# Kernel tuning notes

Measured on AMD Instinct MI355X. Metric: run time of the kernel, lower is better.

## Reference

```python
import jax, jax.numpy as jnp
import numpy as np

N_NODES = 50000
N_EDGES = 1600000
IN_DIM = 512
OUT_DIM = 256


def setup_inputs() -> dict:
    key = jax.random.key(0)
    k1, k2, k3, k4, k5, k6 = jax.random.split(key, 6)
    inputs = jax.random.normal(k1, (N_NODES, IN_DIM), dtype=jnp.float32)
    edge_row = jax.random.randint(k2, (N_EDGES,), 0, N_NODES, dtype=jnp.int32)
    edge_col = jax.random.randint(k3, (N_EDGES,), 0, N_NODES, dtype=jnp.int32)
    edge_val = jax.random.uniform(k4, (N_EDGES,), dtype=jnp.float32)
    stdv = 1.0 / np.sqrt(OUT_DIM)
    weight = jax.random.uniform(k5, (IN_DIM, OUT_DIM), dtype=jnp.float32, minval=-stdv, maxval=stdv)
    bias = jax.random.uniform(k6, (OUT_DIM,), dtype=jnp.float32, minval=-stdv, maxval=stdv)
    return {"inputs": inputs, "edge_row": edge_row, "edge_col": edge_col,
            "edge_val": edge_val, "weight": weight, "bias": bias}


def reference(inputs, edge_row, edge_col, edge_val, weight, bias):
    # dense GEMM: [N, in] @ [in, out] -> [N, out]
    support = inputs @ weight
    # SpMM: out[r] += val * support[c] for each edge (r, c, val)
    gathered = edge_val[:, None] * support[edge_col]  # [E, out]
    output = jax.ops.segment_sum(gathered, edge_row, num_segments=N_NODES)
    return output + bias
```

## Files before the change

kernel.cpp:

```cpp
#include <hip/hip_runtime.h>

#define N_NODES 50000
#define N_EDGES 1600000
#define IN_DIM 512
#define OUT_DIM 256

#define BM 64
#define BN 256
#define BK 32
#define APAD 8
#define LDA (BK + APAD)

#define RPB   128
#define NBKT  391
#define CHUNK 4096
#define CAP   5120

typedef unsigned int u32;
typedef unsigned short u16;
typedef short bf16x8 __attribute__((ext_vector_type(8)));
typedef float f32x4 __attribute__((ext_vector_type(4)));

__device__ __forceinline__ float bf_to_f(u16 u) { return __uint_as_float(((u32)u) << 16); }
__device__ __forceinline__ u16 f_to_bf(float f) {
    u32 u = __float_as_uint(f);
    u32 r = (u + 0x7fffu + ((u >> 16) & 1u)) >> 16;
    return (u16)r;
}

__global__ __launch_bounds__(256) void scatter1(const int* __restrict__ er,
                                                const int* __restrict__ ec,
                                                const float* __restrict__ ev,
                                                int* __restrict__ cursor,
                                                int2* __restrict__ tmp) {
    __shared__ int  hcnt[NBKT];
    __shared__ int  loff[NBKT];
    __shared__ int  gbase[NBKT];
    __shared__ int  sc[512];
    __shared__ int2 estage[CHUNK];
    __shared__ u16  bslot[CHUNK];

    const int t = threadIdx.x;
    const int base = blockIdx.x * CHUNK;
    const int nedge = min(CHUNK, N_EDGES - base);

    for (int k = t; k < NBKT; k += 256) hcnt[k] = 0;
    __syncthreads();

    int w0[16], w1[16], rk[16];
    #pragma unroll
    for (int j = 0; j < 16; ++j) {
        const int i = j * 256 + t;
        rk[j] = -1;
        if (i < nedge) {
            const int e = base + i;
            const int r = er[e];
            const int bk = r >> 7;
            w0[j] = ec[e] | ((r & 127) << 16) | (bk << 23);
            w1[j] = __float_as_int(ev[e]);
            rk[j] = atomicAdd(&hcnt[bk], 1);
        }
    }
    __syncthreads();

    sc[t]       = (t < NBKT) ? hcnt[t] : 0;
    sc[t + 256] = (t + 256 < NBKT) ? hcnt[t + 256] : 0;
    __syncthreads();
    #pragma unroll
    for (int off = 1; off < 512; off <<= 1) {
        const int a0 = (t >= off) ? sc[t - off] : 0;
        const int a1 = sc[t + 256 - off];
        __syncthreads();
        sc[t] += a0;
        sc[t + 256] += a1;
        __syncthreads();
    }
    if (t < NBKT)       loff[t]       = sc[t] - hcnt[t];
    if (t + 256 < NBKT) loff[t + 256] = sc[t + 256] - hcnt[t + 256];

    if (t < NBKT && hcnt[t] > 0)
        gbase[t] = t * CAP + atomicAdd(&cursor[t], hcnt[t]);
    if (t + 256 < NBKT && hcnt[t + 256] > 0)
        gbase[t + 256] = (t + 256) * CAP + atomicAdd(&cursor[t + 256], hcnt[t + 256]);
    __syncthreads();

    #pragma unroll
    for (int j = 0; j < 16; ++j) {
        if (rk[j] >= 0) {
            const int bk = ((u32)w0[j]) >> 23;
            const int s = loff[bk] + rk[j];
            estage[s] = make_int2(w0[j], w1[j]);
            bslot[s]  = (u16)bk;
        }
    }
    __syncthreads();

    for (int s = t; s < nedge; s += 256) {
        const int bk = bslot[s];
        const int2 e2 = estage[s];
        const int gpos = gbase[bk] + (s - loff[bk]);
        if (gpos < (bk + 1) * CAP)
            tmp[gpos] = e2;
    }
}

__global__ __launch_bounds__(256) void scatter2(const int* __restrict__ cursor,
                                                const int2* __restrict__ tmp,
                                                int* __restrict__ row_ptr,
                                                int2* __restrict__ sedge) {
    __shared__ int sc[512];
    __shared__ int orig[512];
    __shared__ int rcnt[RPB];
    __shared__ int rsc[RPB];
    __shared__ int rcur[RPB];
    const int t = threadIdx.x;
    const int b = blockIdx.x;

    const int c0 = (t < NBKT) ? min(cursor[t], CAP) : 0;
    const int c1 = (t + 256 < NBKT) ? min(cursor[t + 256], CAP) : 0;
    sc[t] = c0;       orig[t] = c0;
    sc[t + 256] = c1; orig[t + 256] = c1;
    __syncthreads();
    #pragma unroll
    for (int off = 1; off < 512; off <<= 1) {
        const int a0 = (t >= off) ? sc[t - off] : 0;
        const int a1 = sc[t + 256 - off];
        __syncthreads();
        sc[t] += a0;
        sc[t + 256] += a1;
        __syncthreads();
    }
    const int gb = sc[b] - orig[b];
    const int n  = orig[b];
    const int2* src = tmp + (size_t)b * CAP;

    if (b == 0 && t == 0) row_ptr[N_NODES] = N_EDGES;

    if (t < RPB) rcnt[t] = 0;
    __syncthreads();
    for (int i = t; i < n; i += 256)
        atomicAdd(&rcnt[(((u32)src[i].x) >> 16) & 127], 1);
    __syncthreads();

    if (t < RPB) rsc[t] = rcnt[t];
    __syncthreads();
    #pragma unroll
    for (int off = 1; off < RPB; off <<= 1) {
        int a = 0;
        if (t < RPB && t >= off) a = rsc[t - off];
        __syncthreads();
        if (t < RPB) rsc[t] += a;
        __syncthreads();
    }
    if (t < RPB) {
        const int excl = rsc[t] - rcnt[t];
        rcur[t] = gb + excl;
        const int row = b * RPB + t;
        if (row < N_NODES) row_ptr[row] = gb + excl;
    }
    __syncthreads();

    for (int i = t; i < n; i += 256) {
        const int2 e2 = src[i];
        const int rloc = (((u32)e2.x) >> 16) & 127;
        const int pos = atomicAdd(&rcur[rloc], 1);
        sedge[pos] = make_int2(e2.x & 0xFFFF, e2.y);
    }
}

__global__ __launch_bounds__(256) void wcvt_zero(const float* __restrict__ W,
                                                 u16* __restrict__ WT,
                                                 int* __restrict__ cursor) {
    if (blockIdx.x < 2) {
        const int i = blockIdx.x * 256 + threadIdx.x;
        if (i < NBKT) cursor[i] = 0;
    }
    const int n  = threadIdx.x;
    const int k0 = blockIdx.x * 4;
    ushort4 o;
    o.x = f_to_bf(W[(size_t)(k0 + 0) * OUT_DIM + n]);
    o.y = f_to_bf(W[(size_t)(k0 + 1) * OUT_DIM + n]);
    o.z = f_to_bf(W[(size_t)(k0 + 2) * OUT_DIM + n]);
    o.w = f_to_bf(W[(size_t)(k0 + 3) * OUT_DIM + n]);
    *(ushort4*)(WT + (size_t)n * IN_DIM + k0) = o;
}

__global__ __launch_bounds__(256) void gemm_mfma(const float* __restrict__ X,
                                                 const u16* __restrict__ WT,
                                                 u16* __restrict__ Sb) {
    __shared__ u16 As[BM * LDA];
    __shared__ u16 Bs[BN * LDA];

    const int tid  = threadIdx.x;
    const int wave = tid >> 6;
    const int lane = tid & 63;
    const int r0   = blockIdx.x * BM;
    const int wn   = wave * 64;
    const int l15  = lane & 15;
    const int quad = lane >> 4;

    f32x4 acc[4][4];
    #pragma unroll
    for (int i = 0; i < 4; ++i)
        #pragma unroll
        for (int j = 0; j < 4; ++j) acc[i][j] = (f32x4)0.f;

    const int arow = tid >> 2;
    const int akp  = (tid & 3) * 8;
    const int xrow = min(r0 + arow, N_NODES - 1);
    const float* xsrc = X + (size_t)xrow * IN_DIM + akp;
    const int brow = tid >> 1;
    const int bkp  = (tid & 1) * 16;
    const u16* bsrc  = WT + (size_t)brow * IN_DIM + bkp;
    const u16* bsrc2 = bsrc + (size_t)128 * IN_DIM;

    float4 fA0 = *(const float4*)(xsrc + 0);
    float4 fA1 = *(const float4*)(xsrc + 4);
    uint4  rB0 = *(const uint4*)(bsrc + 0);
    uint4  rB1 = *(const uint4*)(bsrc + 8);
    uint4  rB2 = *(const uint4*)(bsrc2 + 0);
    uint4  rB3 = *(const uint4*)(bsrc2 + 8);

    for (int kc = 0; kc < IN_DIM; kc += BK) {
        {
            ushort4 p0, p1;
            p0.x = f_to_bf(fA0.x); p0.y = f_to_bf(fA0.y); p0.z = f_to_bf(fA0.z); p0.w = f_to_bf(fA0.w);
            p1.x = f_to_bf(fA1.x); p1.y = f_to_bf(fA1.y); p1.z = f_to_bf(fA1.z); p1.w = f_to_bf(fA1.w);
            *(ushort4*)&As[arow * LDA + akp + 0] = p0;
            *(ushort4*)&As[arow * LDA + akp + 4] = p1;
            *(uint4*)&Bs[brow * LDA + bkp + 0] = rB0;
            *(uint4*)&Bs[brow * LDA + bkp + 8] = rB1;
            *(uint4*)&Bs[(brow + 128) * LDA + bkp + 0] = rB2;
            *(uint4*)&Bs[(brow + 128) * LDA + bkp + 8] = rB3;
        }
        __syncthreads();

        if (kc + BK < IN_DIM) {
            fA0 = *(const float4*)(xsrc + kc + BK + 0);
            fA1 = *(const float4*)(xsrc + kc + BK + 4);
            rB0 = *(const uint4*)(bsrc + kc + BK + 0);
            rB1 = *(const uint4*)(bsrc + kc + BK + 8);
            rB2 = *(const uint4*)(bsrc2 + kc + BK + 0);
            rB3 = *(const uint4*)(bsrc2 + kc + BK + 8);
        }

        bf16x8 af[4], bfr[4];
        #pragma unroll
        for (int mt = 0; mt < 4; ++mt)
            af[mt] = *(const bf16x8*)&As[(mt * 16 + l15) * LDA + quad * 8];
        #pragma unroll
        for (int nt = 0; nt < 4; ++nt)
            bfr[nt] = *(const bf16x8*)&Bs[(wn + nt * 16 + l15) * LDA + quad * 8];
        #pragma unroll
        for (int mt = 0; mt < 4; ++mt)
            #pragma unroll
            for (int nt = 0; nt < 4; ++nt)
                acc[mt][nt] = __builtin_amdgcn_mfma_f32_16x16x32_bf16(
                    af[mt], bfr[nt], acc[mt][nt], 0, 0, 0);
        __syncthreads();
    }

    #pragma unroll
    for (int mt = 0; mt < 4; ++mt) {
        #pragma unroll
        for (int r = 0; r < 4; ++r) {
            const int grow = r0 + mt * 16 + quad * 4 + r;
            if (grow < N_NODES) {
                u16* dst = Sb + (size_t)grow * OUT_DIM + wn + l15;
                #pragma unroll
                for (int nt = 0; nt < 4; ++nt)
                    dst[nt * 16] = f_to_bf(acc[mt][nt][r]);
            }
        }
    }
}

__global__ __launch_bounds__(256) void csr_spmm(const int* __restrict__ row_ptr,
                                                const int2* __restrict__ sedge,
                                                const u16* __restrict__ Sb,
                                                const float* __restrict__ bias,
                                                float* __restrict__ out,
                                                int rbase) {
    const int wave = threadIdx.x >> 6;
    const int lane = threadIdx.x & 63;
    const int r = rbase + blockIdx.x * 4 + wave;
    if (r >= N_NODES) return;

    const int start = row_ptr[r];
    const int end   = row_ptr[r + 1];

    float4 acc = *(const float4*)(bias + lane * 4);
    const u16* sbase = Sb + lane * 4;

    int e = start;
    for (; e + 16 <= end; e += 16) {
        int2 ed[16];
        #pragma unroll
        for (int j = 0; j < 16; ++j) ed[j] = sedge[e + j];

        ushort4 sv[16];
        #pragma unroll
        for (int j = 0; j < 16; ++j)
            sv[j] = *(const ushort4*)(sbase + (size_t)ed[j].x * OUT_DIM);

        #pragma unroll
        for (int j = 0; j < 16; ++j) {
            const float vj = __int_as_float(ed[j].y);
            acc.x += vj * bf_to_f(sv[j].x);
            acc.y += vj * bf_to_f(sv[j].y);
            acc.z += vj * bf_to_f(sv[j].z);
            acc.w += vj * bf_to_f(sv[j].w);
        }
    }
    if (e < end) {
        int2 ed[16];
        #pragma unroll
        for (int j = 0; j < 16; ++j)
            ed[j] = sedge[min(e + j, end - 1)];
        #pragma unroll
        for (int j = 0; j < 16; ++j)
            if (e + j >= end) ed[j].y = 0;

        ushort4 sv[16];
        #pragma unroll
        for (int j = 0; j < 16; ++j)
            sv[j] = *(const ushort4*)(sbase + (size_t)ed[j].x * OUT_DIM);

        #pragma unroll
        for (int j = 0; j < 16; ++j) {
            const float vj = __int_as_float(ed[j].y);
            acc.x += vj * bf_to_f(sv[j].x);
            acc.y += vj * bf_to_f(sv[j].y);
            acc.z += vj * bf_to_f(sv[j].z);
            acc.w += vj * bf_to_f(sv[j].w);
        }
    }

    *(float4*)(out + (size_t)r * OUT_DIM + lane * 4) = acc;
}

extern "C" void kernel_launch(void* const* d_in, const int* in_sizes, int n_in,
                              void* d_out, int out_size, void* d_ws, size_t ws_size,
                              hipStream_t stream) {
    const float* X    = (const float*)d_in[0];
    const int*   er   = (const int*)d_in[1];
    const int*   ec   = (const int*)d_in[2];
    const float* ev   = (const float*)d_in[3];
    const float* W    = (const float*)d_in[4];
    const float* bias = (const float*)d_in[5];
    float* out        = (float*)d_out;

    char* ws = (char*)d_ws;
    u16*  Sb      = (u16*) (ws);
    int2* tmp     = (int2*)(ws);
    int*  cursor  = (int*) (ws + 16100000);
    int2* sedge   = (int2*)(ws + 25600000);
    u16*  WT      = (u16*) (ws + 38400000);
    int*  row_ptr = (int*) (ws + 38662144);

    hipLaunchKernelGGL(wcvt_zero, dim3(IN_DIM / 4), dim3(256), 0, stream,
                       W, WT, cursor);
    hipLaunchKernelGGL(scatter1, dim3((N_EDGES + CHUNK - 1) / CHUNK), dim3(256), 0,
                       stream, er, ec, ev, cursor, tmp);
    hipLaunchKernelGGL(scatter2, dim3(NBKT), dim3(256), 0, stream,
                       cursor, tmp, row_ptr, sedge);
    hipLaunchKernelGGL(gemm_mfma, dim3((N_NODES + BM - 1) / BM), dim3(256), 0,
                       stream, X, WT, Sb);
    hipLaunchKernelGGL(csr_spmm, dim3(25000 / 4), dim3(256), 0, stream,
                       row_ptr, sedge, Sb, bias, out, 0);
    hipLaunchKernelGGL(csr_spmm, dim3(25000 / 4), dim3(256), 0, stream,
                       row_ptr, sedge, Sb, bias, out, 25000);
}
```

Baseline: 357.0 us.

## Fuse CSR bucket sort pass with GEMM in one heterogeneous launch

Merges the second scatter kernel (per-bucket row sort and row_ptr build) and the bf16 MFMA GEMM into one grid. The first NBKT blocks do the sort and the rest do GEMM tiles, so the two independent stages can overlap and one launch boundary disappears. Because tmp previously aliased the Sb buffer, the workspace is relaid out so tmp, WT, row_ptr and cursor no longer overlap Sb. The cost is a larger workspace footprint and shared memory sized for the GEMM in every block.

```diff
diff --git a/kernel.cpp b/kernel.cpp
--- a/kernel.cpp
+++ b/kernel.cpp
@@ -14,6 +14,7 @@
 #define RPB   128
 #define NBKT  391
 #define CHUNK 4096
+#define EPT   16
 #define CAP   5120
 
 typedef unsigned int u32;
@@ -47,9 +48,9 @@
     for (int k = t; k < NBKT; k += 256) hcnt[k] = 0;
     __syncthreads();
 
-    int w0[16], w1[16], rk[16];
+    int w0[EPT], w1[EPT], rk[EPT];
     #pragma unroll
-    for (int j = 0; j < 16; ++j) {
+    for (int j = 0; j < EPT; ++j) {
         const int i = j * 256 + t;
         rk[j] = -1;
         if (i < nedge) {
@@ -85,7 +86,7 @@
     __syncthreads();
 
     #pragma unroll
-    for (int j = 0; j < 16; ++j) {
+    for (int j = 0; j < EPT; ++j) {
         if (rk[j] >= 0) {
             const int bk = ((u32)w0[j]) >> 23;
             const int s = loff[bk] + rk[j];
@@ -101,70 +102,6 @@
         const int gpos = gbase[bk] + (s - loff[bk]);
         if (gpos < (bk + 1) * CAP)
             tmp[gpos] = e2;
-    }
-}
-
-__global__ __launch_bounds__(256) void scatter2(const int* __restrict__ cursor,
-                                                const int2* __restrict__ tmp,
-                                                int* __restrict__ row_ptr,
-                                                int2* __restrict__ sedge) {
-    __shared__ int sc[512];
-    __shared__ int orig[512];
-    __shared__ int rcnt[RPB];
-    __shared__ int rsc[RPB];
-    __shared__ int rcur[RPB];
-    const int t = threadIdx.x;
-    const int b = blockIdx.x;
-
-    const int c0 = (t < NBKT) ? min(cursor[t], CAP) : 0;
-    const int c1 = (t + 256 < NBKT) ? min(cursor[t + 256], CAP) : 0;
-    sc[t] = c0;       orig[t] = c0;
-    sc[t + 256] = c1; orig[t + 256] = c1;
-    __syncthreads();
-    #pragma unroll
-    for (int off = 1; off < 512; off <<= 1) {
-        const int a0 = (t >= off) ? sc[t - off] : 0;
-        const int a1 = sc[t + 256 - off];
-        __syncthreads();
-        sc[t] += a0;
-        sc[t + 256] += a1;
-        __syncthreads();
-    }
-    const int gb = sc[b] - orig[b];
-    const int n  = orig[b];
-    const int2* src = tmp + (size_t)b * CAP;
-
-    if (b == 0 && t == 0) row_ptr[N_NODES] = N_EDGES;
-
-    if (t < RPB) rcnt[t] = 0;
-    __syncthreads();
-    for (int i = t; i < n; i += 256)
-        atomicAdd(&rcnt[(((u32)src[i].x) >> 16) & 127], 1);
-    __syncthreads();
-
-    if (t < RPB) rsc[t] = rcnt[t];
-    __syncthreads();
-    #pragma unroll
-    for (int off = 1; off < RPB; off <<= 1) {
-        int a = 0;
-        if (t < RPB && t >= off) a = rsc[t - off];
-        __syncthreads();
-        if (t < RPB) rsc[t] += a;
-        __syncthreads();
-    }
-    if (t < RPB) {
-        const int excl = rsc[t] - rcnt[t];
-        rcur[t] = gb + excl;
-        const int row = b * RPB + t;
-        if (row < N_NODES) row_ptr[row] = gb + excl;
-    }
-    __syncthreads();
-
-    for (int i = t; i < n; i += 256) {
-        const int2 e2 = src[i];
-        const int rloc = (((u32)e2.x) >> 16) & 127;
-        const int pos = atomicAdd(&rcur[rloc], 1);
-        sedge[pos] = make_int2(e2.x & 0xFFFF, e2.y);
     }
 }
 
@@ -185,91 +122,158 @@
     *(ushort4*)(WT + (size_t)n * IN_DIM + k0) = o;
 }
 
-__global__ __launch_bounds__(256) void gemm_mfma(const float* __restrict__ X,
-                                                 const u16* __restrict__ WT,
-                                                 u16* __restrict__ Sb) {
-    __shared__ u16 As[BM * LDA];
-    __shared__ u16 Bs[BN * LDA];
-
-    const int tid  = threadIdx.x;
-    const int wave = tid >> 6;
-    const int lane = tid & 63;
-    const int r0   = blockIdx.x * BM;
-    const int wn   = wave * 64;
-    const int l15  = lane & 15;
-    const int quad = lane >> 4;
-
-    f32x4 acc[4][4];
-    #pragma unroll
-    for (int i = 0; i < 4; ++i)
-        #pragma unroll
-        for (int j = 0; j < 4; ++j) acc[i][j] = (f32x4)0.f;
-
-    const int arow = tid >> 2;
-    const int akp  = (tid & 3) * 8;
-    const int xrow = min(r0 + arow, N_NODES - 1);
-    const float* xsrc = X + (size_t)xrow * IN_DIM + akp;
-    const int brow = tid >> 1;
-    const int bkp  = (tid & 1) * 16;
-    const u16* bsrc  = WT + (size_t)brow * IN_DIM + bkp;
-    const u16* bsrc2 = bsrc + (size_t)128 * IN_DIM;
-
-    float4 fA0 = *(const float4*)(xsrc + 0);
-    float4 fA1 = *(const float4*)(xsrc + 4);
-    uint4  rB0 = *(const uint4*)(bsrc + 0);
-    uint4  rB1 = *(const uint4*)(bsrc + 8);
-    uint4  rB2 = *(const uint4*)(bsrc2 + 0);
-    uint4  rB3 = *(const uint4*)(bsrc2 + 8);
-
-    for (int kc = 0; kc < IN_DIM; kc += BK) {
-        {
-            ushort4 p0, p1;
-            p0.x = f_to_bf(fA0.x); p0.y = f_to_bf(fA0.y); p0.z = f_to_bf(fA0.z); p0.w = f_to_bf(fA0.w);
-            p1.x = f_to_bf(fA1.x); p1.y = f_to_bf(fA1.y); p1.z = f_to_bf(fA1.z); p1.w = f_to_bf(fA1.w);
-            *(ushort4*)&As[arow * LDA + akp + 0] = p0;
-            *(ushort4*)&As[arow * LDA + akp + 4] = p1;
-            *(uint4*)&Bs[brow * LDA + bkp + 0] = rB0;
-            *(uint4*)&Bs[brow * LDA + bkp + 8] = rB1;
-            *(uint4*)&Bs[(brow + 128) * LDA + bkp + 0] = rB2;
-            *(uint4*)&Bs[(brow + 128) * LDA + bkp + 8] = rB3;
-        }
-        __syncthreads();
-
-        if (kc + BK < IN_DIM) {
-            fA0 = *(const float4*)(xsrc + kc + BK + 0);
-            fA1 = *(const float4*)(xsrc + kc + BK + 4);
-            rB0 = *(const uint4*)(bsrc + kc + BK + 0);
-            rB1 = *(const uint4*)(bsrc + kc + BK + 8);
-            rB2 = *(const uint4*)(bsrc2 + kc + BK + 0);
-            rB3 = *(const uint4*)(bsrc2 + kc + BK + 8);
-        }
-
-        bf16x8 af[4], bfr[4];
-        #pragma unroll
-        for (int mt = 0; mt < 4; ++mt)
-            af[mt] = *(const bf16x8*)&As[(mt * 16 + l15) * LDA + quad * 8];
-        #pragma unroll
-        for (int nt = 0; nt < 4; ++nt)
-            bfr[nt] = *(const bf16x8*)&Bs[(wn + nt * 16 + l15) * LDA + quad * 8];
-        #pragma unroll
-        for (int mt = 0; mt < 4; ++mt)
+__global__ __launch_bounds__(256) void fused_s2_gemm(const int* __restrict__ cursor,
+                                                     const int2* __restrict__ tmp,
+                                                     int* __restrict__ row_ptr,
+                                                     int2* __restrict__ sedge,
+                                                     const float* __restrict__ X,
+                                                     const u16* __restrict__ WT,
+                                                     u16* __restrict__ Sb) {
+    __shared__ __align__(16) char smem[BM * LDA * 2 + BN * LDA * 2];
+
+    const int t = threadIdx.x;
+
+    if (blockIdx.x < NBKT) {
+        int* sc   = (int*)smem;
+        int* orig = sc + 512;
+        int* rcnt = orig + 512;
+        int* rsc  = rcnt + RPB;
+        int* rcur = rsc + RPB;
+        const int b = blockIdx.x;
+
+        const int c0 = (t < NBKT) ? min(cursor[t], CAP) : 0;
+        const int c1 = (t + 256 < NBKT) ? min(cursor[t + 256], CAP) : 0;
+        sc[t] = c0;       orig[t] = c0;
+        sc[t + 256] = c1; orig[t + 256] = c1;
+        __syncthreads();
+        #pragma unroll
+        for (int off = 1; off < 512; off <<= 1) {
+            const int a0 = (t >= off) ? sc[t - off] : 0;
+            const int a1 = sc[t + 256 - off];
+            __syncthreads();
+            sc[t] += a0;
+            sc[t + 256] += a1;
+            __syncthreads();
+        }
+        const int gb = sc[b] - orig[b];
+        const int n  = orig[b];
+        const int2* src = tmp + (size_t)b * CAP;
+
+        if (b == 0 && t == 0) row_ptr[N_NODES] = N_EDGES;
+
+        if (t < RPB) rcnt[t] = 0;
+        __syncthreads();
+        for (int i = t; i < n; i += 256)
+            atomicAdd(&rcnt[(((u32)src[i].x) >> 16) & 127], 1);
+        __syncthreads();
+
+        if (t < RPB) rsc[t] = rcnt[t];
+        __syncthreads();
+        #pragma unroll
+        for (int off = 1; off < RPB; off <<= 1) {
+            int a = 0;
+            if (t < RPB && t >= off) a = rsc[t - off];
+            __syncthreads();
+            if (t < RPB) rsc[t] += a;
+            __syncthreads();
+        }
+        if (t < RPB) {
+            const int excl = rsc[t] - rcnt[t];
+            rcur[t] = gb + excl;
+            const int row = b * RPB + t;
+            if (row < N_NODES) row_ptr[row] = gb + excl;
+        }
+        __syncthreads();
+
+        for (int i = t; i < n; i += 256) {
+            const int2 e2 = src[i];
+            const int rloc = (((u32)e2.x) >> 16) & 127;
+            const int pos = atomicAdd(&rcur[rloc], 1);
+            sedge[pos] = make_int2(e2.x & 0xFFFF, e2.y);
+        }
+    } else {
+        u16* As = (u16*)smem;
+        u16* Bs = (u16*)(smem + BM * LDA * 2);
+
+        const int wave = t >> 6;
+        const int lane = t & 63;
+        const int r0   = (blockIdx.x - NBKT) * BM;
+        const int wn   = wave * 64;
+        const int l15  = lane & 15;
+        const int quad = lane >> 4;
+
+        f32x4 acc[4][4];
+        #pragma unroll
+        for (int i = 0; i < 4; ++i)
+            #pragma unroll
+            for (int j = 0; j < 4; ++j) acc[i][j] = (f32x4)0.f;
+
+        const int arow = t >> 2;
+        const int akp  = (t & 3) * 8;
+        const int xrow = min(r0 + arow, N_NODES - 1);
+        const float* xsrc = X + (size_t)xrow * IN_DIM + akp;
+        const int brow = t >> 1;
+        const int bkp  = (t & 1) * 16;
+        const u16* bsrc  = WT + (size_t)brow * IN_DIM + bkp;
+        const u16* bsrc2 = bsrc + (size_t)128 * IN_DIM;
+
+        float4 fA0 = *(const float4*)(xsrc + 0);
+        float4 fA1 = *(const float4*)(xsrc + 4);
+        uint4  rB0 = *(const uint4*)(bsrc + 0);
+        uint4  rB1 = *(const uint4*)(bsrc + 8);
+        uint4  rB2 = *(const uint4*)(bsrc2 + 0);
+        uint4  rB3 = *(const uint4*)(bsrc2 + 8);
+
+        for (int kc = 0; kc < IN_DIM; kc += BK) {
+            {
+                ushort4 p0, p1;
+                p0.x = f_to_bf(fA0.x); p0.y = f_to_bf(fA0.y); p0.z = f_to_bf(fA0.z); p0.w = f_to_bf(fA0.w);
+                p1.x = f_to_bf(fA1.x); p1.y = f_to_bf(fA1.y); p1.z = f_to_bf(fA1.z); p1.w = f_to_bf(fA1.w);
+                *(ushort4*)&As[arow * LDA + akp + 0] = p0;
+                *(ushort4*)&As[arow * LDA + akp + 4] = p1;
+                *(uint4*)&Bs[brow * LDA + bkp + 0] = rB0;
+                *(uint4*)&Bs[brow * LDA + bkp + 8] = rB1;
+                *(uint4*)&Bs[(brow + 128) * LDA + bkp + 0] = rB2;
+                *(uint4*)&Bs[(brow + 128) * LDA + bkp + 8] = rB3;
+            }
+            __syncthreads();
+
+            if (kc + BK < IN_DIM) {
+                fA0 = *(const float4*)(xsrc + kc + BK + 0);
+                fA1 = *(const float4*)(xsrc + kc + BK + 4);
+                rB0 = *(const uint4*)(bsrc + kc + BK + 0);
+                rB1 = *(const uint4*)(bsrc + kc + BK + 8);
+                rB2 = *(const uint4*)(bsrc2 + kc + BK + 0);
+                rB3 = *(const uint4*)(bsrc2 + kc + BK + 8);
+            }
+
+            bf16x8 af[4], bfr[4];
+            #pragma unroll
+            for (int mt = 0; mt < 4; ++mt)
+                af[mt] = *(const bf16x8*)&As[(mt * 16 + l15) * LDA + quad * 8];
             #pragma unroll
             for (int nt = 0; nt < 4; ++nt)
-                acc[mt][nt] = __builtin_amdgcn_mfma_f32_16x16x32_bf16(
-                    af[mt], bfr[nt], acc[mt][nt], 0, 0, 0);
-        __syncthreads();
-    }
-
-    #pragma unroll
-    for (int mt = 0; mt < 4; ++mt) {
-        #pragma unroll
-        for (int r = 0; r < 4; ++r) {
-            const int grow = r0 + mt * 16 + quad * 4 + r;
-            if (grow < N_NODES) {
-                u16* dst = Sb + (size_t)grow * OUT_DIM + wn + l15;
+                bfr[nt] = *(const bf16x8*)&Bs[(wn + nt * 16 + l15) * LDA + quad * 8];
+            #pragma unroll
+            for (int mt = 0; mt < 4; ++mt)
                 #pragma unroll
                 for (int nt = 0; nt < 4; ++nt)
-                    dst[nt * 16] = f_to_bf(acc[mt][nt][r]);
+                    acc[mt][nt] = __builtin_amdgcn_mfma_f32_16x16x32_bf16(
+                        af[mt], bfr[nt], acc[mt][nt], 0, 0, 0);
+            __syncthreads();
+        }
+
+        #pragma unroll
+        for (int mt = 0; mt < 4; ++mt) {
+            #pragma unroll
+            for (int r = 0; r < 4; ++r) {
+                const int grow = r0 + mt * 16 + quad * 4 + r;
+                if (grow < N_NODES) {
+                    u16* dst = Sb + (size_t)grow * OUT_DIM + wn + l15;
+                    #pragma unroll
+                    for (int nt = 0; nt < 4; ++nt)
+                        dst[nt * 16] = f_to_bf(acc[mt][nt][r]);
+                }
             }
         }
     }
@@ -352,20 +356,19 @@
 
     char* ws = (char*)d_ws;
     u16*  Sb      = (u16*) (ws);
-    int2* tmp     = (int2*)(ws);
-    int*  cursor  = (int*) (ws + 16100000);
     int2* sedge   = (int2*)(ws + 25600000);
-    u16*  WT      = (u16*) (ws + 38400000);
-    int*  row_ptr = (int*) (ws + 38662144);
+    int2* tmp     = (int2*)(ws + 38400000);
+    u16*  WT      = (u16*) (ws + 54415360);
+    int*  row_ptr = (int*) (ws + 54677504);
+    int*  cursor  = (int*) (ws + 54877508);
 
     hipLaunchKernelGGL(wcvt_zero, dim3(IN_DIM / 4), dim3(256), 0, stream,
                        W, WT, cursor);
     hipLaunchKernelGGL(scatter1, dim3((N_EDGES + CHUNK - 1) / CHUNK), dim3(256), 0,
                        stream, er, ec, ev, cursor, tmp);
-    hipLaunchKernelGGL(scatter2, dim3(NBKT), dim3(256), 0, stream,
-                       cursor, tmp, row_ptr, sedge);
-    hipLaunchKernelGGL(gemm_mfma, dim3((N_NODES + BM - 1) / BM), dim3(256), 0,
-                       stream, X, WT, Sb);
+    hipLaunchKernelGGL(fused_s2_gemm, dim3(NBKT + (N_NODES + BM - 1) / BM),
+                       dim3(256), 0, stream,
+                       cursor, tmp, row_ptr, sedge, X, WT, Sb);
     hipLaunchKernelGGL(csr_spmm, dim3(25000 / 4), dim3(256), 0, stream,
                        row_ptr, sedge, Sb, bias, out, 0);
     hipLaunchKernelGGL(csr_spmm, dim3(25000 / 4), dim3(256), 0, stream,
```

Result: no change. 360.5 us (+1.0%).
